# Performance work log

Hardware: AMD Instinct MI355X
Metric: run time of the kernel (lower is better)

The kernel has to match this reference:

```python
import jax, jax.numpy as jnp
import numpy as np

T, X_D, M_N, CHUNK, REDUCE = 2048, 2048, 64, 64, 8
M_D = X_D // REDUCE          # 256
DECAY_D = M_D // 4           # 64
H_D = X_D * 2                # factor=2
FF_D = 256 * round(int(H_D * (2.0 / 3.0)) / 256)  # 2816


def setup_inputs() -> dict:
    key = jax.random.key(0)
    ks = jax.random.split(key, 20)
    def lin(k, out_d, in_d):
        return (jax.random.normal(k, (out_d, in_d), jnp.float32) / np.sqrt(in_d).astype(np.float32))
    return {
        "xs": jax.random.normal(ks[0], (T, X_D), jnp.float32),
        "attn_q": lin(ks[1], X_D // REDUCE, X_D),
        "attn_k": lin(ks[2], X_D // REDUCE, X_D // REDUCE),
        "attn_v": lin(ks[3], X_D, X_D),
        "attn_o": lin(ks[4], X_D, X_D),
        "attn_r": lin(ks[5], X_D, X_D),
        "mem_f": lin(ks[6], M_N, X_D),
        "mem_q": lin(ks[7], M_D, X_D),
        "mem_k": lin(ks[8], M_D, M_D),
        "mem_v": lin(ks[9], M_D, X_D),
        "mem_o": lin(ks[10], X_D, M_D),
        "mem_r": lin(ks[11], X_D, X_D),
        "mem_beta": -jnp.ones((M_N, M_D), jnp.float32),
        "mem_decay": 3.0 * jnp.ones((M_N, DECAY_D), jnp.float32),
        "mem_l": jax.random.uniform(ks[12], (M_N, M_D), dtype=jnp.float32),
        "ff_in1": lin(ks[13], FF_D, X_D),
        "ff_in2": lin(ks[14], FF_D, X_D),
        "ff_out": lin(ks[15], X_D, FF_D),
        "sn1_g": jnp.sqrt(jnp.float32(X_D)),
        "sn2_g": jnp.sqrt(jnp.float32(X_D)),
    }


def _rotate_half(x):
    x1 = x[..., ::2]
    x2 = x[..., 1::2]
    return jnp.stack((-x2, x1), axis=-1).reshape(x.shape)


def _scale_norm(x, g):
    return x * (g / (jnp.linalg.norm(x, axis=-1, keepdims=True) + 1e-8))


def _attn(xs, Wq, Wk, Wv, Wo, Wr):
    n = CHUNK
    q = xs @ Wq.T                       # (T, dk)
    k = q @ Wk.T                        # k is computed from q (as in source)
    v = xs @ Wv.T                       # (T, x_d)
    c = xs.shape[0] // n
    dk = q.shape[-1]
    q = q.reshape(c, n, dk)
    k = k.reshape(c, n, dk)
    v = v.reshape(c, n, v.shape[-1])

    def with_prev(a):                   # prepend previous chunk (zero for chunk 0)
        prev = jnp.concatenate([jnp.zeros_like(a[:1]), a[:-1]], axis=0)
        return jnp.concatenate([prev, a], axis=1)   # (c, 2n, d)

    k2, v2 = with_prev(k), with_prev(v)

    # RoPE over 2n key positions; queries take the last n positions
    inv_freq = 1.0 / (10000.0 ** (jnp.arange(0, dk, 2, dtype=jnp.float32) / dk))
    ang = jnp.arange(2 * n, dtype=jnp.float32)[:, None] * inv_freq[None, :]
    sin = jnp.repeat(jnp.sin(ang), 2, axis=-1)      # (2n, dk) interleaved
    cos = jnp.repeat(jnp.cos(ang), 2, axis=-1)
    q = q * cos[None, n:] + _rotate_half(q) * sin[None, n:]
    k2 = k2 * cos[None] + _rotate_half(k2) * sin[None]

    qk = jnp.einsum('cnk,cmk->cnm', q, k2) / jnp.sqrt(jnp.float32(dk))
    allowed = jnp.arange(2 * n)[None, :] <= (jnp.arange(n)[:, None] + n)  # tril offset n
    A = jax.nn.softmax(jnp.where(allowed[None], qk, -jnp.inf), axis=-1)
    y = jnp.einsum('cnm,cmv->cnv', A, v2).reshape(xs.shape[0], -1)
    return (y @ Wo.T) * jax.nn.sigmoid(xs @ Wr.T)


def _mem(xs, Wf, Wq, Wk, Wv, Wo, Wr, beta_p, decay_p, l_p):
    v = xs @ Wv.T                                       # (T, m_d)
    f = jax.nn.sigmoid(xs @ Wf.T)[:, :, None]           # (T, m_n, 1)
    beta = jax.nn.sigmoid(beta_p)[None]                 # (1, m_n, m_d)
    gamma = jnp.concatenate(
        [jnp.ones((M_N, M_D - DECAY_D), xs.dtype), jax.nn.sigmoid(decay_p)], axis=1
    )[None]                                             # (1, m_n, m_d)
    ws = (1.0 - f * beta) * gamma                       # (T, m_n, m_d)
    fvs = f * v[:, None, :]                             # (T, m_n, m_d)

    def bin_assoc(ei, ej):
        ai, bi = ei
        aj, bj = ej
        return (aj * ai, aj * bi + bj)

    _, mems = jax.lax.associative_scan(bin_assoc, (ws, fvs), axis=0)  # (T, m_n, m_d)

    q = xs @ Wq.T                                       # (T, m_d)
    k = jnp.einsum('nmd,kd->nmk', mems, Wk) + l_p[None]
    A = jax.nn.softmax(jnp.einsum('nmk,nk->nm', k, q) / jnp.sqrt(jnp.float32(M_D)), axis=-1)
    y = jnp.einsum('nm,nmd->nd', A, mems)
    return (y @ Wo.T) * jax.nn.sigmoid(xs @ Wr.T)


def _ff(xs, W1, W2, Wo):
    return (jax.nn.silu(xs @ W1.T) * (xs @ W2.T)) @ Wo.T


def reference(xs, attn_q, attn_k, attn_v, attn_o, attn_r,
              mem_f, mem_q, mem_k, mem_v, mem_o, mem_r,
              mem_beta, mem_decay, mem_l,
              ff_in1, ff_in2, ff_out, sn1_g, sn2_g):
    xn = _scale_norm(xs, sn1_g)
    xs = (_attn(xn, attn_q, attn_k, attn_v, attn_o, attn_r)
          + _mem(xn, mem_f, mem_q, mem_k, mem_v, mem_o, mem_r, mem_beta, mem_decay, mem_l)
          + xs)
    xs = _ff(_scale_norm(xs, sn2_g), ff_in1, ff_in2, ff_out) + xs
    return xs
```

## Files before the change

### kernel.cpp

```cpp
#include <hip/hip_runtime.h>
#include <math.h>


typedef short bhalf8 __attribute__((ext_vector_type(8)));
typedef float f32x4 __attribute__((ext_vector_type(4)));

#define CC_LD 7168
#define COL_V   0
#define COL_B1  2048
#define COL_B2  4096
#define COL_QB  6144
#define COL_VM  6400
#define COL_QM  6656
#define COL_FG  6912

#define AS1 __attribute__((address_space(1)))
#define AS3 __attribute__((address_space(3)))

__device__ __forceinline__ float sigmoidf_(float x){ return 1.0f/(1.0f+expf(-x)); }

__device__ __forceinline__ unsigned short f2b(float f){
  unsigned u = __float_as_uint(f);
  unsigned r = (u + 0x7fffu + ((u>>16)&1u)) >> 16;
  return (unsigned short)r;
}
__device__ __forceinline__ float b2f(unsigned short h){
  return __uint_as_float(((unsigned)h)<<16);
}

__global__ void k_f2b_all(
    const float* __restrict__ av, const float* __restrict__ ar, const float* __restrict__ mr,
    const float* __restrict__ aq, const float* __restrict__ mv, const float* __restrict__ mq,
    const float* __restrict__ mf, const float* __restrict__ ao, const float* __restrict__ mo,
    const float* __restrict__ f1, const float* __restrict__ f2, const float* __restrict__ fo,
    const float* __restrict__ ak,
    unsigned short* __restrict__ WCAT, unsigned short* __restrict__ AOB,
    unsigned short* __restrict__ MOB, unsigned short* __restrict__ FFW,
    unsigned short* __restrict__ FFOB, unsigned short* __restrict__ AKB){
  int i = blockIdx.x*256 + threadIdx.x;
  const float* s; unsigned short* d; int off;
  if (i < 3571712){
    d = WCAT + (size_t)i*4;
    if      (i < 1048576){ s = av; off = i; }
    else if (i < 2097152){ s = ar; off = i-1048576; }
    else if (i < 3145728){ s = mr; off = i-2097152; }
    else if (i < 3276800){ s = aq; off = i-3145728; }
    else if (i < 3407872){ s = mv; off = i-3276800; }
    else if (i < 3538944){ s = mq; off = i-3407872; }
    else                 { s = mf; off = i-3538944; }
  }
  else if (i < 4620288){ off = i-3571712; s = ao; d = AOB  + (size_t)off*4; }
  else if (i < 4751360){ off = i-4620288; s = mo; d = MOB  + (size_t)off*4; }
  else if (i < 6193152){ off = i-4751360; s = f1;
    int row = off >> 9, c4 = off & 511;
    d = FFW + ((size_t)row*2)*2048 + c4*4; }
  else if (i < 7634944){ off = i-6193152; s = f2;
    int row = off >> 9, c4 = off & 511;
    d = FFW + ((size_t)row*2 + 1)*2048 + c4*4; }
  else if (i < 9076736){ off = i-7634944; s = fo; d = FFOB + (size_t)off*4; }
  else if (i < 9093120){ off = i-9076736; s = ak; d = AKB  + (size_t)off*4; }
  else return;
  float4 v = ((const float4*)s)[off];
  ushort4 o;
  o.x = f2b(v.x); o.y = f2b(v.y); o.z = f2b(v.z); o.w = f2b(v.w);
  *(ushort4*)d = o;
}

__global__ void k_f2bT(const float* __restrict__ s, unsigned short* __restrict__ d){
  int i = blockIdx.x, j = threadIdx.x;
  d[(size_t)j*256 + i] = f2b(s[(size_t)i*256 + j]);
}

__global__ void k_trig(float2* __restrict__ TR){
  int idx = blockIdx.x*256 + threadIdx.x;
  int pos = idx >> 7, j = idx & 127;
  float inv = powf(10000.f, -(float)j/128.f);
  float a = (float)pos * inv;
  TR[idx] = make_float2(cosf(a), sinf(a));
}

__global__ __launch_bounds__(256) void k_scalenorm_b(const float* __restrict__ x,
    const float* __restrict__ g, unsigned short* __restrict__ ob){
  int row = blockIdx.x, tid = threadIdx.x;
  const float* xr = x + (size_t)row*2048;
  float ss = 0.f;
  for (int j = tid; j < 2048; j += 256){ float v = xr[j]; ss += v*v; }
  __shared__ float red[256];
  red[tid] = ss; __syncthreads();
  for (int s = 128; s > 0; s >>= 1){ if (tid < s) red[tid] += red[tid+s]; __syncthreads(); }
  float scale = g[0] / (sqrtf(red[0]) + 1e-8f);
  unsigned short* orow = ob + (size_t)row*2048;
  for (int j4 = tid; j4 < 512; j4 += 256){
    float4 v = *(const float4*)(xr + j4*4);
    ushort4 o;
    o.x = f2b(v.x*scale); o.y = f2b(v.y*scale); o.z = f2b(v.z*scale); o.w = f2b(v.w*scale);
    ((ushort4*)orow)[j4] = o;
  }
}

__global__ __launch_bounds__(512) void k_gemm_big(
    const unsigned short* __restrict__ A, int lda,
    const unsigned short* __restrict__ B,
    unsigned short* __restrict__ Cb, int K, int ldc, int epi, int gate_ld){
  __shared__ unsigned short LDSu[49152];
  int tid = threadIdx.x;
  int w = tid >> 6, l = tid & 63;
  int bi = blockIdx.y, bj = blockIdx.x;
  int m0 = bi*256, n0 = bj*256;
  int wr = w >> 2, wc = w & 3;

  f32x4 acc[8][4];
#pragma unroll
  for (int i=0;i<8;++i)
#pragma unroll
    for (int j=0;j<4;++j){ f32x4 z = {0.f,0.f,0.f,0.f}; acc[i][j] = z; }

  const int r0 = tid >> 2;
  const int gsrc8 = (((tid&3) ^ ((tid>>3)&3)) * 8);

  auto stage = [&](int bs, int kt){
    unsigned short* db = LDSu + bs*16384;
    const unsigned short* ap0 = A + (size_t)(m0 + r0)*lda       + kt*32 + gsrc8;
    const unsigned short* ap1 = A + (size_t)(m0 + 128 + r0)*lda + kt*32 + gsrc8;
    const unsigned short* bp0 = B + (size_t)(n0 + r0)*K         + kt*32 + gsrc8;
    const unsigned short* bp1 = B + (size_t)(n0 + 128 + r0)*K   + kt*32 + gsrc8;
    __builtin_amdgcn_global_load_lds((const AS1 void*)ap0, (AS3 void*)(db + tid*8),         16, 0, 0);
    __builtin_amdgcn_global_load_lds((const AS1 void*)ap1, (AS3 void*)(db + 4096 + tid*8),  16, 0, 0);
    __builtin_amdgcn_global_load_lds((const AS1 void*)bp0, (AS3 void*)(db + 8192 + tid*8),  16, 0, 0);
    __builtin_amdgcn_global_load_lds((const AS1 void*)bp1, (AS3 void*)(db + 12288 + tid*8), 16, 0, 0);
  };

  const int nt = K >> 5;
  stage(0, 0);
  stage(1, 1);
  asm volatile("s_waitcnt vmcnt(4)" ::: "memory");
  __builtin_amdgcn_s_barrier();

  const int lr = l & 15;
  const int gsw = (((l>>4) ^ ((l>>1)&3)) * 8);
  const int aoff = (wr*128 + lr)*32 + gsw;
  const int boff = 8192 + (wc*64 + lr)*32 + gsw;

  int cur = 0;
  for (int t = 0; t < nt; ++t){
    if (t + 2 < nt) stage((t+2)%3, t+2);
    const unsigned short* Tb = LDSu + cur*16384;
    bhalf8 bfr[4];
#pragma unroll
    for (int n=0;n<4;++n) bfr[n] = *(const bhalf8*)(Tb + boff + n*512);
    __builtin_amdgcn_s_setprio(1);
#pragma unroll
    for (int fr=0;fr<8;++fr){
      bhalf8 af = *(const bhalf8*)(Tb + aoff + fr*512);
#pragma unroll
      for (int n=0;n<4;++n)
        acc[fr][n] = __builtin_amdgcn_mfma_f32_16x16x32_bf16(af, bfr[n], acc[fr][n], 0, 0, 0);
    }
    __builtin_amdgcn_s_setprio(0);
    if (t + 1 < nt){
      if (t + 2 < nt){ asm volatile("s_waitcnt vmcnt(4)" ::: "memory"); }
      else           { asm volatile("s_waitcnt vmcnt(0)" ::: "memory"); }
      __builtin_amdgcn_s_barrier();
      cur = (cur == 2) ? 0 : cur + 1;
    }
  }

#pragma unroll
  for (int fr=0;fr<8;++fr){
    int rowb = m0 + wr*128 + fr*16 + ((l>>4)<<2);
#pragma unroll
    for (int r=0;r<4;++r){
      int row = rowb + r;
      size_t rbase = (size_t)row*ldc;
      size_t gbase = (size_t)row*gate_ld;
#pragma unroll
      for (int n=0;n<4;++n){
        int col = n0 + wc*64 + n*16 + (l&15);
        float v = acc[fr][n][r];
        if (epi == 4){
          float o = __shfl_xor(v, 1);
          if ((l & 1) == 0)
            Cb[gbase + (col>>1)] = f2b(v*sigmoidf_(v)*o);
        } else {
          Cb[rbase + col] = f2b(v);
        }
      }
    }
  }
}

__global__ __launch_bounds__(256) void k_gemm_p(
    const unsigned short* __restrict__ A, int lda,
    const unsigned short* __restrict__ B,
    float* __restrict__ C, unsigned short* __restrict__ Cb,
    int N, int K, int ldc, int epi,
    const float* __restrict__ add,
    const unsigned short* __restrict__ gate, int gate_ld,
    const unsigned short* A2, const unsigned short* B2, float* C2){
  __shared__ unsigned short LDSu[24576];
  int tid = threadIdx.x;
  int w = tid >> 6, l = tid & 63;
  int bi = blockIdx.y, bj = blockIdx.x;
  const unsigned short* Ap = A; const unsigned short* Bp = B; float* Cp = C;
  if (blockIdx.z){ Ap = A2; Bp = B2; Cp = C2; }
  int m0 = bi*128, n0 = bj*128;
  int wr = w >> 1, wc = w & 1;

  f32x4 acc[4][4];
#pragma unroll
  for (int i=0;i<4;++i)
#pragma unroll
    for (int j=0;j<4;++j){ f32x4 z = {0.f,0.f,0.f,0.f}; acc[i][j] = z; }

  const int r0 = tid >> 2;
  const int gsrc8 = (((tid&3) ^ ((tid>>3)&3)) * 8);

  auto stage = [&](int bs, int kt){
    unsigned short* db = LDSu + bs*8192;
    const unsigned short* ap0 = Ap + (size_t)(m0 + r0)*lda      + kt*32 + gsrc8;
    const unsigned short* ap1 = Ap + (size_t)(m0 + 64 + r0)*lda + kt*32 + gsrc8;
    const unsigned short* bp0 = Bp + (size_t)(n0 + r0)*K        + kt*32 + gsrc8;
    const unsigned short* bp1 = Bp + (size_t)(n0 + 64 + r0)*K   + kt*32 + gsrc8;
    __builtin_amdgcn_global_load_lds((const AS1 void*)ap0, (AS3 void*)(db + tid*8),        16, 0, 0);
    __builtin_amdgcn_global_load_lds((const AS1 void*)ap1, (AS3 void*)(db + 2048 + tid*8), 16, 0, 0);
    __builtin_amdgcn_global_load_lds((const AS1 void*)bp0, (AS3 void*)(db + 4096 + tid*8), 16, 0, 0);
    __builtin_amdgcn_global_load_lds((const AS1 void*)bp1, (AS3 void*)(db + 6144 + tid*8), 16, 0, 0);
  };

  const int nt = K >> 5;
  stage(0, 0);
  stage(1, 1);
  asm volatile("s_waitcnt vmcnt(4)" ::: "memory");
  __builtin_amdgcn_s_barrier();

  const int lr = l & 15;
  const int gsw = (((l>>4) ^ ((l>>1)&3)) * 8);
  const int aoff = (wr*64 + lr)*32 + gsw;
  const int boff = 4096 + (wc*64 + lr)*32 + gsw;

  int cur = 0;
  for (int t = 0; t < nt; ++t){
    if (t + 2 < nt) stage((t+2)%3, t+2);
    const unsigned short* Tb = LDSu + cur*8192;
    bhalf8 af[4], bfr[4];
#pragma unroll
    for (int m=0;m<4;++m) af[m]  = *(const bhalf8*)(Tb + aoff + m*512);
#pragma unroll
    for (int n=0;n<4;++n) bfr[n] = *(const bhalf8*)(Tb + boff + n*512);
    __builtin_amdgcn_s_setprio(1);
#pragma unroll
    for (int m=0;m<4;++m)
#pragma unroll
      for (int n=0;n<4;++n)
        acc[m][n] = __builtin_amdgcn_mfma_f32_16x16x32_bf16(af[m], bfr[n], acc[m][n], 0, 0, 0);
    __builtin_amdgcn_s_setprio(0);
    if (t + 1 < nt){
      if (t + 2 < nt){ asm volatile("s_waitcnt vmcnt(4)" ::: "memory"); }
      else           { asm volatile("s_waitcnt vmcnt(0)" ::: "memory"); }
      __builtin_amdgcn_s_barrier();
      cur = (cur == 2) ? 0 : cur + 1;
    }
  }

#pragma unroll
  for (int m=0;m<4;++m){
    int rowb = m0 + wr*64 + m*16 + ((l>>4)<<2);
#pragma unroll
    for (int r=0;r<4;++r){
      int row = rowb + r;
      size_t rbase = (size_t)row*ldc;
      size_t gbase = (size_t)row*gate_ld;
#pragma unroll
      for (int n=0;n<4;++n){
        int col = n0 + wc*64 + n*16 + (l&15);
        float v = acc[m][n][r];
        if (add) v += add[rbase + col];
        if (epi == 2) v *= sigmoidf_(b2f(gate[gbase + col]));
        if (epi == 3) Cb[rbase + col] = f2b(v);
        else          Cp[rbase + col] = v;
      }
    }
  }
}

__global__ __launch_bounds__(256) void k_gemm_fuse2(
    const unsigned short* __restrict__ A,  const unsigned short* __restrict__ B,
    const unsigned short* __restrict__ A2, const unsigned short* __restrict__ B2,
    const unsigned short* __restrict__ gate1, const unsigned short* __restrict__ gate2,
    const float* __restrict__ xs, float* __restrict__ XS2){
  __shared__ unsigned short LDSu[24576];
  int tid = threadIdx.x;
  int w = tid >> 6, l = tid & 63;
  int bi = blockIdx.y, bj = blockIdx.x;
  int m0 = bi*128, n0 = bj*128;
  int wr = w >> 1, wc = w & 1;

  f32x4 acc[4][4], acc2[4][4];
#pragma unroll
  for (int i=0;i<4;++i)
#pragma unroll
    for (int j=0;j<4;++j){ f32x4 z = {0.f,0.f,0.f,0.f}; acc[i][j] = z; acc2[i][j] = z; }

  const int r0 = tid >> 2;
  const int gsrc8 = (((tid&3) ^ ((tid>>3)&3)) * 8);

  auto stage = [&](int bs, int kt, const unsigned short* Ap, int lda,
                   const unsigned short* Bp, int ldb){
    unsigned short* db = LDSu + bs*8192;
    const unsigned short* ap0 = Ap + (size_t)(m0 + r0)*lda      + kt*32 + gsrc8;
    const unsigned short* ap1 = Ap + (size_t)(m0 + 64 + r0)*lda + kt*32 + gsrc8;
    const unsigned short* bp0 = Bp + (size_t)(n0 + r0)*ldb      + kt*32 + gsrc8;
    const unsigned short* bp1 = Bp + (size_t)(n0 + 64 + r0)*ldb + kt*32 + gsrc8;
    __builtin_amdgcn_global_load_lds((const AS1 void*)ap0, (AS3 void*)(db + tid*8),        16, 0, 0);
    __builtin_amdgcn_global_load_lds((const AS1 void*)ap1, (AS3 void*)(db + 2048 + tid*8), 16, 0, 0);
    __builtin_amdgcn_global_load_lds((const AS1 void*)bp0, (AS3 void*)(db + 4096 + tid*8), 16, 0, 0);
    __builtin_amdgcn_global_load_lds((const AS1 void*)bp1, (AS3 void*)(db + 6144 + tid*8), 16, 0, 0);
  };

  const int lr = l & 15;
  const int gsw = (((l>>4) ^ ((l>>1)&3)) * 8);
  const int aoff = (wr*64 + lr)*32 + gsw;
  const int boff = 4096 + (wc*64 + lr)*32 + gsw;

  {
    const int nt = 64;
    stage(0, 0, A, 2048, B, 2048);
    stage(1, 1, A, 2048, B, 2048);
    asm volatile("s_waitcnt vmcnt(4)" ::: "memory");
    __builtin_amdgcn_s_barrier();
    int cur = 0;
    for (int t = 0; t < nt; ++t){
      if (t + 2 < nt) stage((t+2)%3, t+2, A, 2048, B, 2048);
      const unsigned short* Tb = LDSu + cur*8192;
      bhalf8 af[4], bfr[4];
#pragma unroll
      for (int m=0;m<4;++m) af[m]  = *(const bhalf8*)(Tb + aoff + m*512);
#pragma unroll
      for (int n=0;n<4;++n) bfr[n] = *(const bhalf8*)(Tb + boff + n*512);
      __builtin_amdgcn_s_setprio(1);
#pragma unroll
      for (int m=0;m<4;++m)
#pragma unroll
        for (int n=0;n<4;++n)
          acc[m][n] = __builtin_amdgcn_mfma_f32_16x16x32_bf16(af[m], bfr[n], acc[m][n], 0, 0, 0);
      __builtin_amdgcn_s_setprio(0);
      if (t + 1 < nt){
        if (t + 2 < nt){ asm volatile("s_waitcnt vmcnt(4)" ::: "memory"); }
        else           { asm volatile("s_waitcnt vmcnt(0)" ::: "memory"); }
        __builtin_amdgcn_s_barrier();
        cur = (cur == 2) ? 0 : cur + 1;
      }
    }
  }
  __syncthreads();

  {
    const int nt = 8;
    stage(0, 0, A2, 256, B2, 256);
    stage(1, 1, A2, 256, B2, 256);
    asm volatile("s_waitcnt vmcnt(4)" ::: "memory");
    __builtin_amdgcn_s_barrier();
    int cur = 0;
    for (int t = 0; t < nt; ++t){
      if (t + 2 < nt) stage((t+2)%3, t+2, A2, 256, B2, 256);
      const unsigned short* Tb = LDSu + cur*8192;
      bhalf8 af[4], bfr[4];
#pragma unroll
      for (int m=0;m<4;++m) af[m]  = *(const bhalf8*)(Tb + aoff + m*512);
#pragma unroll
      for (int n=0;n<4;++n) bfr[n] = *(const bhalf8*)(Tb + boff + n*512);
      __builtin_amdgcn_s_setprio(1);
#pragma unroll
      for (int m=0;m<4;++m)
#pragma unroll
        for (int n=0;n<4;++n)
          acc2[m][n] = __builtin_amdgcn_mfma_f32_16x16x32_bf16(af[m], bfr[n], acc2[m][n], 0, 0, 0);
      __builtin_amdgcn_s_setprio(0);
      if (t + 1 < nt){
        if (t + 2 < nt){ asm volatile("s_waitcnt vmcnt(4)" ::: "memory"); }
        else           { asm volatile("s_waitcnt vmcnt(0)" ::: "memory"); }
        __builtin_amdgcn_s_barrier();
        cur = (cur == 2) ? 0 : cur + 1;
      }
    }
  }

#pragma unroll
  for (int m=0;m<4;++m){
    int rowb = m0 + wr*64 + m*16 + ((l>>4)<<2);
#pragma unroll
    for (int r=0;r<4;++r){
      int row = rowb + r;
      size_t gb = (size_t)row*CC_LD;
      size_t rb = (size_t)row*2048;
#pragma unroll
      for (int n=0;n<4;++n){
        int col = n0 + wc*64 + n*16 + (l&15);
        float v = acc[m][n][r]*sigmoidf_(b2f(gate1[gb + col]))
                + acc2[m][n][r]*sigmoidf_(b2f(gate2[gb + col]))
                + xs[rb + col];
        XS2[rb + col] = v;
      }
    }
  }
}

__global__ __launch_bounds__(256) void k_attn_scores_mfma(
    const unsigned short* __restrict__ CCqb, const float* __restrict__ K0,
    const float2* __restrict__ TR, unsigned short* __restrict__ P){
  __shared__ unsigned short Ks[128*256];
  int c = blockIdx.x, tid = threadIdx.x;
  for (int it = 0; it < 16; ++it){
    int id = tid + it*256;
    int m = id >> 5;
    int cs = (id & 31) * 8;
    float v[8];
    if (c == 0 && m < 64){
#pragma unroll
      for (int u=0;u<8;++u) v[u] = 0.f;
    } else {
      int gr = (c-1)*64 + m;
      const float* kr = K0 + (size_t)gr*256 + cs;
      float4 x0 = *(const float4*)kr, x1 = *(const float4*)(kr+4);
      v[0]=x0.x; v[1]=x0.y; v[2]=x0.z; v[3]=x0.w;
      v[4]=x1.x; v[5]=x1.y; v[6]=x1.z; v[7]=x1.w;
#pragma unroll
      for (int p2=0;p2<4;++p2){
        float2 t = TR[m*128 + (cs>>1) + p2];
        float e = v[2*p2], o = v[2*p2+1];
        v[2*p2]   = e*t.x - o*t.y;
        v[2*p2+1] = o*t.x + e*t.y;
      }
    }
    unsigned short pk[8];
#pragma unroll
    for (int u=0;u<8;++u) pk[u] = f2b(v[u]);
    int byte = m*512 + ((cs*2) ^ ((m&7)<<4));
    *(bhalf8*)((char*)&Ks[0] + byte) = *(const bhalf8*)pk;
  }
  __syncthreads();

  int w = tid >> 6, l = tid & 63;
  int lr = l & 15, lkg = l >> 4;
  f32x4 acc[8];
#pragma unroll
  for (int n=0;n<8;++n){ f32x4 z = {0.f,0.f,0.f,0.f}; acc[n] = z; }

  int iq = w*16 + lr;
  const unsigned short* qbase = CCqb + (size_t)(c*64 + iq)*CC_LD;
  int pos = 64 + iq;

  for (int kt = 0; kt < 8; ++kt){
    int k0c = kt*32 + lkg*8;
    bhalf8 q8 = *(const bhalf8*)(qbase + k0c);
    float v[8];
#pragma unroll
    for (int u=0;u<8;++u) v[u] = b2f((unsigned short)(((short*)&q8)[u]));
#pragma unroll
    for (int p2=0;p2<4;++p2){
      float2 t = TR[pos*128 + (k0c>>1) + p2];
      float e = v[2*p2], o = v[2*p2+1];
      v[2*p2]   = e*t.x - o*t.y;
      v[2*p2+1] = o*t.x + e*t.y;
    }
    unsigned short pk[8];
#pragma unroll
    for (int u=0;u<8;++u) pk[u] = f2b(v[u]);
    bhalf8 af = *(const bhalf8*)pk;
#pragma unroll
    for (int n=0;n<8;++n){
      int m = n*16 + lr;
      int byte = m*512 + ((k0c*2) ^ ((m&7)<<4));
      bhalf8 bf = *(const bhalf8*)((const char*)&Ks[0] + byte);
      acc[n] = __builtin_amdgcn_mfma_f32_16x16x32_bf16(af, bf, acc[n], 0, 0, 0);
    }
  }

  int i0 = w*16 + lkg*4;
  float mx[4] = {-1e30f,-1e30f,-1e30f,-1e30f};
  float sm[4] = {0.f,0.f,0.f,0.f};
#pragma unroll
  for (int n=0;n<8;++n){
    int col = n*16 + lr;
#pragma unroll
    for (int r=0;r<4;++r){
      float vv = acc[n][r] * (1.f/16.f);
      if (col > i0 + r + 64) vv = -1e30f;
      acc[n][r] = vv;
      mx[r] = fmaxf(mx[r], vv);
    }
  }
#pragma unroll
  for (int s=1; s<16; s<<=1)
#pragma unroll
    for (int r=0;r<4;++r) mx[r] = fmaxf(mx[r], __shfl_xor(mx[r], s));
#pragma unroll
  for (int n=0;n<8;++n)
#pragma unroll
    for (int r=0;r<4;++r){
      float e = expf(acc[n][r] - mx[r]);
      acc[n][r] = e; sm[r] += e;
    }
#pragma unroll
  for (int s=1; s<16; s<<=1)
#pragma unroll
    for (int r=0;r<4;++r) sm[r] += __shfl_xor(sm[r], s);
  float rcp[4];
#pragma unroll
  for (int r=0;r<4;++r) rcp[r] = 1.f/sm[r];

  unsigned short* Pr = P + (size_t)c*8192;
#pragma unroll
  for (int n=0;n<8;++n){
    int col = n*16 + lr;
#pragma unroll
    for (int r=0;r<4;++r)
      Pr[(i0+r)*128 + col] = f2b(acc[n][r]*rcp[r]);
  }
}

__global__ __launch_bounds__(256) void k_attn_pv_mfma(
    const unsigned short* __restrict__ P, const unsigned short* __restrict__ Vb, int vld,
    unsigned short* __restrict__ Y){
  __shared__ unsigned short Vt[128*128];
  int ct = blockIdx.x, c = blockIdx.y, tid = threadIdx.x;
  {
    int k = tid >> 1;
    int ch = (tid & 1) * 64;
    if (c == 0 && k < 64){
      for (int u=0; u<64; ++u){
        int col = ch + u;
        int byte = col*256 + ((k*2) ^ ((col&7)<<4));
        *(unsigned short*)((char*)&Vt[0] + byte) = 0;
      }
    } else {
      int gr = (c-1)*64 + k;
      const unsigned short* vr = Vb + (size_t)gr*vld + ct*128 + ch;
      for (int u8=0; u8<8; ++u8){
        bhalf8 x = *(const bhalf8*)(vr + u8*8);
#pragma unroll
        for (int u=0;u<8;++u){
          int col = ch + u8*8 + u;
          int byte = col*256 + ((k*2) ^ ((col&7)<<4));
          *(unsigned short*)((char*)&Vt[0] + byte) = (unsigned short)(((short*)&x)[u]);
        }
      }
    }
  }
  __syncthreads();
  int w = tid >> 6, l = tid & 63, lr = l & 15, lkg = l >> 4;
  f32x4 acc[8];
#pragma unroll
  for (int n=0;n<8;++n){ f32x4 z = {0.f,0.f,0.f,0.f}; acc[n] = z; }
  const unsigned short* Pr = P + (size_t)c*8192;
  for (int kt=0; kt<4; ++kt){
    int kb = kt*32 + lkg*8;
    bhalf8 af = *(const bhalf8*)(Pr + (w*16 + lr)*128 + kb);
#pragma unroll
    for (int n=0;n<8;++n){
      int col = n*16 + lr;
      int byte = col*256 + ((kb*2) ^ ((col&7)<<4));
      bhalf8 bf = *(const bhalf8*)((const char*)&Vt[0] + byte);
      acc[n] = __builtin_amdgcn_mfma_f32_16x16x32_bf16(af, bf, acc[n], 0, 0, 0);
    }
  }
  int row0 = c*64 + w*16 + lkg*4;
#pragma unroll
  for (int n=0;n<8;++n){
    int col = ct*128 + n*16 + lr;
#pragma unroll
    for (int r=0;r<4;++r)
      Y[(size_t)(row0+r)*2048 + col] = f2b(acc[n][r]);
  }
}

__global__ __launch_bounds__(256) void k_scan1(const unsigned short* __restrict__ CC,
    const float* __restrict__ beta_p, const float* __restrict__ decay_p,
    float* __restrict__ CP, float* __restrict__ CQ){
  int c = blockIdx.x, mg = blockIdx.y, d = threadIdx.x;
  __shared__ float Fs[512];
  for (int v = threadIdx.x; v < 512; v += 256){
    int s = v >> 3, j = v & 7;
    Fs[v] = sigmoidf_(b2f(CC[(size_t)(c*64+s)*CC_LD + COL_FG + mg*8 + j]));
  }
  __syncthreads();
  float beta[8], gamma[8], Pa[8], Qa[8];
#pragma unroll
  for (int j=0;j<8;++j){
    int m = mg*8+j;
    beta[j]  = sigmoidf_(beta_p[m*256+d]);
    gamma[j] = (d < 192) ? 1.f : sigmoidf_(decay_p[m*64 + (d-192)]);
    Pa[j] = 1.f; Qa[j] = 0.f;
  }
  for (int s = 0; s < 64; ++s){
    float vm = b2f(CC[(size_t)(c*64+s)*CC_LD + COL_VM + d]);
#pragma unroll
    for (int j=0;j<8;++j){
      float f = Fs[s*8+j];
      float w = (1.f - f*beta[j])*gamma[j];
      Pa[j] *= w;
      Qa[j] = w*Qa[j] + f*vm;
    }
  }
#pragma unroll
  for (int j=0;j<8;++j){
    size_t idx = ((size_t)c*64 + mg*8 + j)*256 + d;
    CP[idx] = Pa[j]; CQ[idx] = Qa[j];
  }
}

__global__ __launch_bounds__(256) void k_scan2(const float* __restrict__ CP,
    const float* __restrict__ CQ, float* __restrict__ SIN){
  int m = blockIdx.x, d = threadIdx.x;
  float S = 0.f;
  for (int c = 0; c < 32; ++c){
    size_t idx = ((size_t)c*64 + m)*256 + d;
    SIN[idx] = S;
    S = CP[idx]*S + CQ[idx];
  }
}

__global__ __launch_bounds__(256) void k_scan3(const unsigned short* __restrict__ CC,
    const float* __restrict__ beta_p, const float* __restrict__ decay_p,
    const float* __restrict__ SIN, unsigned short* __restrict__ MEMS){
  int c = blockIdx.x, mg = blockIdx.y, d = threadIdx.x;
  __shared__ float Fs[512];
  for (int v = threadIdx.x; v < 512; v += 256){
    int s = v >> 3, j = v & 7;
    Fs[v] = sigmoidf_(b2f(CC[(size_t)(c*64+s)*CC_LD + COL_FG + mg*8 + j]));
  }
  __syncthreads();
  float beta[8], gamma[8], S[8];
#pragma unroll
  for (int j=0;j<8;++j){
    int m = mg*8+j;
    beta[j]  = sigmoidf_(beta_p[m*256+d]);
    gamma[j] = (d < 192) ? 1.f : sigmoidf_(decay_p[m*64 + (d-192)]);
    S[j] = SIN[((size_t)c*64 + m)*256 + d];
  }
  for (int s = 0; s < 64; ++s){
    float vm = b2f(CC[(size_t)(c*64+s)*CC_LD + COL_VM + d]);
    size_t tb = (size_t)(c*64+s)*64;
#pragma unroll
    for (int j=0;j<8;++j){
      float f = Fs[s*8+j];
      float w = (1.f - f*beta[j])*gamma[j];
      S[j] = w*S[j] + f*vm;
      MEMS[(tb + mg*8 + j)*256 + d] = f2b(S[j]);
    }
  }
}

__global__ __launch_bounds__(256) void k_memread(const unsigned short* __restrict__ MEMS,
    const float* __restrict__ QH, const unsigned short* __restrict__ QMs, int qm_ld,
    const float* __restrict__ L, unsigned short* __restrict__ YMb){
  int t = blockIdx.x, tid = threadIdx.x;
  int wave = tid >> 6, lane = tid & 63;
  __shared__ float anorm[64];
  const unsigned short* Mt = MEMS + (size_t)t*16384;
  float4 qh4 = *(const float4*)(QH + (size_t)t*256 + lane*4);
  ushort4 qmu = *(const ushort4*)(QMs + (size_t)t*qm_ld + lane*4);
  float qm0 = b2f(qmu.x), qm1 = b2f(qmu.y), qm2 = b2f(qmu.z), qm3 = b2f(qmu.w);
  for (int mi = 0; mi < 16; ++mi){
    int m = wave*16 + mi;
    ushort4 su = *(const ushort4*)(Mt + m*256 + lane*4);
    float4 l4 = *(const float4*)(L + (size_t)m*256 + lane*4);
    float p = b2f(su.x)*qh4.x + b2f(su.y)*qh4.y + b2f(su.z)*qh4.z + b2f(su.w)*qh4.w
            + l4.x*qm0 + l4.y*qm1 + l4.z*qm2 + l4.w*qm3;
#pragma unroll
    for (int off = 32; off > 0; off >>= 1) p += __shfl_down(p, off);
    if (lane == 0) anorm[m] = p * (1.f/16.f);
  }
  __syncthreads();
  if (tid < 64){
    float v = anorm[tid];
    float mx = v;
#pragma unroll
    for (int off = 32; off > 0; off >>= 1) mx = fmaxf(mx, __shfl_xor(mx, off));
    float e = expf(v - mx);
    float s = e;
#pragma unroll
    for (int off = 32; off > 0; off >>= 1) s += __shfl_xor(s, off);
    anorm[tid] = e / s;
  }
  __syncthreads();
  float acc = 0.f;
  for (int m = 0; m < 64; ++m) acc += anorm[m]*b2f(Mt[m*256 + tid]);
  YMb[(size_t)t*256 + tid] = f2b(acc);
}

extern "C" void kernel_launch(void* const* d_in, const int* in_sizes, int n_in,
                              void* d_out, int out_size, void* d_ws, size_t ws_size,
                              hipStream_t stream){
  const float* xs        = (const float*)d_in[0];
  const float* attn_q    = (const float*)d_in[1];
  const float* attn_k    = (const float*)d_in[2];
  const float* attn_v    = (const float*)d_in[3];
  const float* attn_o    = (const float*)d_in[4];
  const float* attn_r    = (const float*)d_in[5];
  const float* mem_f     = (const float*)d_in[6];
  const float* mem_q     = (const float*)d_in[7];
  const float* mem_k     = (const float*)d_in[8];
  const float* mem_v     = (const float*)d_in[9];
  const float* mem_o     = (const float*)d_in[10];
  const float* mem_r     = (const float*)d_in[11];
  const float* mem_beta  = (const float*)d_in[12];
  const float* mem_decay = (const float*)d_in[13];
  const float* mem_l     = (const float*)d_in[14];
  const float* ff1       = (const float*)d_in[15];
  const float* ff2       = (const float*)d_in[16];
  const float* ffo       = (const float*)d_in[17];
  const float* sn1       = (const float*)d_in[18];
  const float* sn2       = (const float*)d_in[19];
  float* out = (float*)d_out;
  float* W = (float*)d_ws;

  unsigned short* XNb  = (unsigned short*)(W + 0);
  unsigned short* WCAT = (unsigned short*)(W + 2097152);
  unsigned short* CCb  = (unsigned short*)(W + 9437184);
  unsigned short* AOB  = (unsigned short*)(W + 16777216);
  unsigned short* MOB  = (unsigned short*)(W + 18874368);
  unsigned short* FFW  = (unsigned short*)(W + 19136512);
  unsigned short* FFOB = (unsigned short*)(W + 24903680);
  unsigned short* AKB  = (unsigned short*)(W + 27787264);
  unsigned short* MKTB = (unsigned short*)(W + 27820032);
  unsigned short* Ybb  = (unsigned short*)(W + 27852800);
  float*          XS2  = W + 34144256;
  unsigned short* MEMSb= (unsigned short*)(W + 38338560);
  float*          CP   = W + 55115776;
  float*          CQ   = W + 55640064;
  float*          SIN  = W + 56164352;
  float2*         TRIG = (float2*)(W + 0);
  float*          K0   = W + 32768;
  unsigned short* P    = (unsigned short*)(W + 557056);
  float*          QH   = W + 688128;
  unsigned short* YMb  = (unsigned short*)(W + 1212416);
  unsigned short* XN2b = MEMSb;
  unsigned short* H1b  = (unsigned short*)(W + 40435712);

  dim3 blk(256);
  dim3 blk512(512);

  k_f2b_all<<<dim3(35520), blk, 0, stream>>>(attn_v, attn_r, mem_r, attn_q, mem_v, mem_q,
      mem_f, attn_o, mem_o, ff1, ff2, ffo, attn_k, WCAT, AOB, MOB, FFW, FFOB, AKB);
  k_f2bT<<<dim3(256), blk, 0, stream>>>(mem_k, MKTB);

  k_scalenorm_b<<<dim3(2048), blk, 0, stream>>>(xs, sn1, XNb);

  k_gemm_big<<<dim3(28, 8), blk512, 0, stream>>>(XNb, 2048, WCAT, CCb, 2048, CC_LD, 3, 0);

  k_trig<<<dim3(64), blk, 0, stream>>>(TRIG);

  k_gemm_p<<<dim3(2, 16, 2), blk, 0, stream>>>(CCb + COL_QB, CC_LD, AKB, K0, nullptr, 256, 256, 256, 0,
      nullptr, nullptr, 0, CCb + COL_QM, MKTB, QH);

  k_attn_scores_mfma<<<dim3(32), blk, 0, stream>>>(CCb + COL_QB, K0, TRIG, P);
  k_attn_pv_mfma<<<dim3(16, 32), blk, 0, stream>>>(P, CCb + COL_V, CC_LD, Ybb);

  k_scan1<<<dim3(32, 8), blk, 0, stream>>>(CCb, mem_beta, mem_decay, CP, CQ);
  k_scan2<<<dim3(64), blk, 0, stream>>>(CP, CQ, SIN);
  k_scan3<<<dim3(32, 8), blk, 0, stream>>>(CCb, mem_beta, mem_decay, SIN, MEMSb);
  k_memread<<<dim3(2048), blk, 0, stream>>>(MEMSb, QH, CCb + COL_QM, CC_LD, mem_l, YMb);

  k_gemm_fuse2<<<dim3(16, 16), blk, 0, stream>>>(Ybb, AOB, YMb, MOB,
      CCb + COL_B1, CCb + COL_B2, xs, XS2);

  k_scalenorm_b<<<dim3(2048), blk, 0, stream>>>(XS2, sn2, XN2b);

  k_gemm_big<<<dim3(22, 8), blk512, 0, stream>>>(XN2b, 2048, FFW, H1b, 2048, 5632, 4, 2816);
  k_gemm_p<<<dim3(16, 16), blk, 0, stream>>>(H1b, 2816, FFOB, out, nullptr, 2048, 2816, 2048, 0,
      XS2, nullptr, 0, nullptr, nullptr, nullptr);
}
```

Baseline: 421.6 us.

## Split GEMM K-step into two phases interleaving A/B prefetch with MFMA halves

Splits each K-iteration of the bf16 MFMA GEMM into two halves. Each half loads a group of A fragments from LDS, issues either the A or the B global-to-LDS prefetch for tile t+2, then runs 16 MFMAs. The aim is to spread global load issue between compute phases, in the style of a ping-pong schedule. It adds three extra workgroup barriers per iteration, which may cost more than the overlap it gains.

```diff
diff --git a/kernel.cpp b/kernel.cpp
--- a/kernel.cpp
+++ b/kernel.cpp
@@ -118,21 +118,24 @@
   const int r0 = tid >> 2;
   const int gsrc8 = (((tid&3) ^ ((tid>>3)&3)) * 8);
 
-  auto stage = [&](int bs, int kt){
+  auto stage_a = [&](int bs, int kt){
     unsigned short* db = LDSu + bs*16384;
     const unsigned short* ap0 = A + (size_t)(m0 + r0)*lda       + kt*32 + gsrc8;
     const unsigned short* ap1 = A + (size_t)(m0 + 128 + r0)*lda + kt*32 + gsrc8;
+    __builtin_amdgcn_global_load_lds((const AS1 void*)ap0, (AS3 void*)(db + tid*8),        16, 0, 0);
+    __builtin_amdgcn_global_load_lds((const AS1 void*)ap1, (AS3 void*)(db + 4096 + tid*8), 16, 0, 0);
+  };
+  auto stage_b = [&](int bs, int kt){
+    unsigned short* db = LDSu + bs*16384;
     const unsigned short* bp0 = B + (size_t)(n0 + r0)*K         + kt*32 + gsrc8;
     const unsigned short* bp1 = B + (size_t)(n0 + 128 + r0)*K   + kt*32 + gsrc8;
-    __builtin_amdgcn_global_load_lds((const AS1 void*)ap0, (AS3 void*)(db + tid*8),         16, 0, 0);
-    __builtin_amdgcn_global_load_lds((const AS1 void*)ap1, (AS3 void*)(db + 4096 + tid*8),  16, 0, 0);
     __builtin_amdgcn_global_load_lds((const AS1 void*)bp0, (AS3 void*)(db + 8192 + tid*8),  16, 0, 0);
     __builtin_amdgcn_global_load_lds((const AS1 void*)bp1, (AS3 void*)(db + 12288 + tid*8), 16, 0, 0);
   };
 
   const int nt = K >> 5;
-  stage(0, 0);
-  stage(1, 1);
+  stage_a(0, 0); stage_b(0, 0);
+  stage_a(1, 1); stage_b(1, 1);
   asm volatile("s_waitcnt vmcnt(4)" ::: "memory");
   __builtin_amdgcn_s_barrier();
 
@@ -143,19 +146,33 @@
 
   int cur = 0;
   for (int t = 0; t < nt; ++t){
-    if (t + 2 < nt) stage((t+2)%3, t+2);
     const unsigned short* Tb = LDSu + cur*16384;
-    bhalf8 bfr[4];
+    bhalf8 bfr[4], af0[4];
 #pragma unroll
     for (int n=0;n<4;++n) bfr[n] = *(const bhalf8*)(Tb + boff + n*512);
+#pragma unroll
+    for (int m=0;m<4;++m) af0[m] = *(const bhalf8*)(Tb + aoff + m*512);
+    if (t + 2 < nt) stage_a((t+2)%3, t+2);
+    __builtin_amdgcn_s_barrier();
     __builtin_amdgcn_s_setprio(1);
 #pragma unroll
-    for (int fr=0;fr<8;++fr){
-      bhalf8 af = *(const bhalf8*)(Tb + aoff + fr*512);
+    for (int m=0;m<4;++m)
 #pragma unroll
       for (int n=0;n<4;++n)
-        acc[fr][n] = __builtin_amdgcn_mfma_f32_16x16x32_bf16(af, bfr[n], acc[fr][n], 0, 0, 0);
-    }
+        acc[m][n] = __builtin_amdgcn_mfma_f32_16x16x32_bf16(af0[m], bfr[n], acc[m][n], 0, 0, 0);
+    __builtin_amdgcn_s_setprio(0);
+    __builtin_amdgcn_s_barrier();
+    bhalf8 af1[4];
+#pragma unroll
+    for (int m=0;m<4;++m) af1[m] = *(const bhalf8*)(Tb + aoff + (m+4)*512);
+    if (t + 2 < nt) stage_b((t+2)%3, t+2);
+    __builtin_amdgcn_s_barrier();
+    __builtin_amdgcn_s_setprio(1);
+#pragma unroll
+    for (int m=0;m<4;++m)
+#pragma unroll
+      for (int n=0;n<4;++n)
+        acc[m+4][n] = __builtin_amdgcn_mfma_f32_16x16x32_bf16(af1[m], bfr[n], acc[m+4][n], 0, 0, 0);
     __builtin_amdgcn_s_setprio(0);
     if (t + 1 < nt){
       if (t + 2 < nt){ asm volatile("s_waitcnt vmcnt(4)" ::: "memory"); }
```

New measurement: 429.0 us. No clear change (+1.8%).

## Replace 256x256 GEMM tiles with 128x128 tiles and add XCD-aware block swizzle

Applied to the files above, without the earlier changes.

Removes the 512-thread 256x256 big-tile GEMM and runs the fused QKV/gate projection and the FF in1/in2 SiLU GEMM with 256-thread 128x128 tiles instead. A new dedicated SiLU-gated kernel takes over the FF case. The launch grids grow fourfold, so more workgroups fill the CUs. A block-index swizzle that groups consecutive tiles onto the same XCD is added to the 128-tile GEMMs to improve L2 locality. In exchange, smaller tiles mean less data reuse per block and more global traffic.

```diff
diff --git a/kernel.cpp b/kernel.cpp
--- a/kernel.cpp
+++ b/kernel.cpp
@@ -26,6 +26,15 @@
 }
 __device__ __forceinline__ float b2f(unsigned short h){
   return __uint_as_float(((unsigned)h)<<16);
+}
+
+__device__ __forceinline__ void xcd_swz(int& bi, int& bj){
+  int gx = gridDim.x;
+  int nwg = gx * gridDim.y;
+  int lin = blockIdx.y * gx + blockIdx.x;
+  int q = nwg >> 3;
+  int swz = (lin & 7) * q + (lin >> 3);
+  bj = swz % gx; bi = swz / gx;
 }
 
 __global__ void k_f2b_all(
@@ -98,97 +107,6 @@
   }
 }
 
-__global__ __launch_bounds__(512) void k_gemm_big(
-    const unsigned short* __restrict__ A, int lda,
-    const unsigned short* __restrict__ B,
-    unsigned short* __restrict__ Cb, int K, int ldc, int epi, int gate_ld){
-  __shared__ unsigned short LDSu[49152];
-  int tid = threadIdx.x;
-  int w = tid >> 6, l = tid & 63;
-  int bi = blockIdx.y, bj = blockIdx.x;
-  int m0 = bi*256, n0 = bj*256;
-  int wr = w >> 2, wc = w & 3;
-
-  f32x4 acc[8][4];
-#pragma unroll
-  for (int i=0;i<8;++i)
-#pragma unroll
-    for (int j=0;j<4;++j){ f32x4 z = {0.f,0.f,0.f,0.f}; acc[i][j] = z; }
-
-  const int r0 = tid >> 2;
-  const int gsrc8 = (((tid&3) ^ ((tid>>3)&3)) * 8);
-
-  auto stage = [&](int bs, int kt){
-    unsigned short* db = LDSu + bs*16384;
-    const unsigned short* ap0 = A + (size_t)(m0 + r0)*lda       + kt*32 + gsrc8;
-    const unsigned short* ap1 = A + (size_t)(m0 + 128 + r0)*lda + kt*32 + gsrc8;
-    const unsigned short* bp0 = B + (size_t)(n0 + r0)*K         + kt*32 + gsrc8;
-    const unsigned short* bp1 = B + (size_t)(n0 + 128 + r0)*K   + kt*32 + gsrc8;
-    __builtin_amdgcn_global_load_lds((const AS1 void*)ap0, (AS3 void*)(db + tid*8),         16, 0, 0);
-    __builtin_amdgcn_global_load_lds((const AS1 void*)ap1, (AS3 void*)(db + 4096 + tid*8),  16, 0, 0);
-    __builtin_amdgcn_global_load_lds((const AS1 void*)bp0, (AS3 void*)(db + 8192 + tid*8),  16, 0, 0);
-    __builtin_amdgcn_global_load_lds((const AS1 void*)bp1, (AS3 void*)(db + 12288 + tid*8), 16, 0, 0);
-  };
-
-  const int nt = K >> 5;
-  stage(0, 0);
-  stage(1, 1);
-  asm volatile("s_waitcnt vmcnt(4)" ::: "memory");
-  __builtin_amdgcn_s_barrier();
-
-  const int lr = l & 15;
-  const int gsw = (((l>>4) ^ ((l>>1)&3)) * 8);
-  const int aoff = (wr*128 + lr)*32 + gsw;
-  const int boff = 8192 + (wc*64 + lr)*32 + gsw;
-
-  int cur = 0;
-  for (int t = 0; t < nt; ++t){
-    if (t + 2 < nt) stage((t+2)%3, t+2);
-    const unsigned short* Tb = LDSu + cur*16384;
-    bhalf8 bfr[4];
-#pragma unroll
-    for (int n=0;n<4;++n) bfr[n] = *(const bhalf8*)(Tb + boff + n*512);
-    __builtin_amdgcn_s_setprio(1);
-#pragma unroll
-    for (int fr=0;fr<8;++fr){
-      bhalf8 af = *(const bhalf8*)(Tb + aoff + fr*512);
-#pragma unroll
-      for (int n=0;n<4;++n)
-        acc[fr][n] = __builtin_amdgcn_mfma_f32_16x16x32_bf16(af, bfr[n], acc[fr][n], 0, 0, 0);
-    }
-    __builtin_amdgcn_s_setprio(0);
-    if (t + 1 < nt){
-      if (t + 2 < nt){ asm volatile("s_waitcnt vmcnt(4)" ::: "memory"); }
-      else           { asm volatile("s_waitcnt vmcnt(0)" ::: "memory"); }
-      __builtin_amdgcn_s_barrier();
-      cur = (cur == 2) ? 0 : cur + 1;
-    }
-  }
-
-#pragma unroll
-  for (int fr=0;fr<8;++fr){
-    int rowb = m0 + wr*128 + fr*16 + ((l>>4)<<2);
-#pragma unroll
-    for (int r=0;r<4;++r){
-      int row = rowb + r;
-      size_t rbase = (size_t)row*ldc;
-      size_t gbase = (size_t)row*gate_ld;
-#pragma unroll
-      for (int n=0;n<4;++n){
-        int col = n0 + wc*64 + n*16 + (l&15);
-        float v = acc[fr][n][r];
-        if (epi == 4){
-          float o = __shfl_xor(v, 1);
-          if ((l & 1) == 0)
-            Cb[gbase + (col>>1)] = f2b(v*sigmoidf_(v)*o);
-        } else {
-          Cb[rbase + col] = f2b(v);
-        }
-      }
-    }
-  }
-}
-
 __global__ __launch_bounds__(256) void k_gemm_p(
     const unsigned short* __restrict__ A, int lda,
     const unsigned short* __restrict__ B,
@@ -200,7 +118,7 @@
   __shared__ unsigned short LDSu[24576];
   int tid = threadIdx.x;
   int w = tid >> 6, l = tid & 63;
-  int bi = blockIdx.y, bj = blockIdx.x;
+  int bi, bj; xcd_swz(bi, bj);
   const unsigned short* Ap = A; const unsigned short* Bp = B; float* Cp = C;
   if (blockIdx.z){ Ap = A2; Bp = B2; Cp = C2; }
   int m0 = bi*128, n0 = bj*128;
@@ -283,6 +201,92 @@
   }
 }
 
+__global__ __launch_bounds__(256) void k_gemm_silu(
+    const unsigned short* __restrict__ A, int lda,
+    const unsigned short* __restrict__ B,
+    unsigned short* __restrict__ Cb, int K, int out_ld){
+  __shared__ unsigned short LDSu[24576];
+  int tid = threadIdx.x;
+  int w = tid >> 6, l = tid & 63;
+  int bi, bj; xcd_swz(bi, bj);
+  int m0 = bi*128, n0 = bj*128;
+  int wr = w >> 1, wc = w & 1;
+
+  f32x4 acc[4][4];
+#pragma unroll
+  for (int i=0;i<4;++i)
+#pragma unroll
+    for (int j=0;j<4;++j){ f32x4 z = {0.f,0.f,0.f,0.f}; acc[i][j] = z; }
+
+  const int r0 = tid >> 2;
+  const int gsrc8 = (((tid&3) ^ ((tid>>3)&3)) * 8);
+
+  auto stage = [&](int bs, int kt){
+    unsigned short* db = LDSu + bs*8192;
+    const unsigned short* ap0 = A + (size_t)(m0 + r0)*lda      + kt*32 + gsrc8;
+    const unsigned short* ap1 = A + (size_t)(m0 + 64 + r0)*lda + kt*32 + gsrc8;
+    const unsigned short* bp0 = B + (size_t)(n0 + r0)*K        + kt*32 + gsrc8;
+    const unsigned short* bp1 = B + (size_t)(n0 + 64 + r0)*K   + kt*32 + gsrc8;
+    __builtin_amdgcn_global_load_lds((const AS1 void*)ap0, (AS3 void*)(db + tid*8),        16, 0, 0);
+    __builtin_amdgcn_global_load_lds((const AS1 void*)ap1, (AS3 void*)(db + 2048 + tid*8), 16, 0, 0);
+    __builtin_amdgcn_global_load_lds((const AS1 void*)bp0, (AS3 void*)(db + 4096 + tid*8), 16, 0, 0);
+    __builtin_amdgcn_global_load_lds((const AS1 void*)bp1, (AS3 void*)(db + 6144 + tid*8), 16, 0, 0);
+  };
+
+  const int nt = K >> 5;
+  stage(0, 0);
+  stage(1, 1);
+  asm volatile("s_waitcnt vmcnt(4)" ::: "memory");
+  __builtin_amdgcn_s_barrier();
+
+  const int lr = l & 15;
+  const int gsw = (((l>>4) ^ ((l>>1)&3)) * 8);
+  const int aoff = (wr*64 + lr)*32 + gsw;
+  const int boff = 4096 + (wc*64 + lr)*32 + gsw;
+
+  int cur = 0;
+  for (int t = 0; t < nt; ++t){
+    if (t + 2 < nt) stage((t+2)%3, t+2);
+    const unsigned short* Tb = LDSu + cur*8192;
+    bhalf8 af[4], bfr[4];
+#pragma unroll
+    for (int m=0;m<4;++m) af[m]  = *(const bhalf8*)(Tb + aoff + m*512);
+#pragma unroll
+    for (int n=0;n<4;++n) bfr[n] = *(const bhalf8*)(Tb + boff + n*512);
+    __builtin_amdgcn_s_setprio(1);
+#pragma unroll
+    for (int m=0;m<4;++m)
+#pragma unroll
+      for (int n=0;n<4;++n)
+        acc[m][n] = __builtin_amdgcn_mfma_f32_16x16x32_bf16(af[m], bfr[n], acc[m][n], 0, 0, 0);
+    __builtin_amdgcn_s_setprio(0);
+    if (t + 1 < nt){
+      if (t + 2 < nt){ asm volatile("s_waitcnt vmcnt(4)" ::: "memory"); }
+      else           { asm volatile("s_waitcnt vmcnt(0)" ::: "memory"); }
+      __builtin_amdgcn_s_barrier();
+      cur = (cur == 2) ? 0 : cur + 1;
+    }
+  }
+
+#pragma unroll
+  for (int m=0;m<4;++m){
+    int rowb = m0 + wr*64 + m*16 + ((l>>4)<<2);
+#pragma unroll
+    for (int r=0;r<4;++r){
+      int row = rowb + r;
+      size_t gbase = (size_t)row*out_ld;
+#pragma unroll
+      for (int n=0;n<4;++n){
+        int col = n0 + wc*64 + n*16 + (l&15);
+        float v = acc[m][n][r];
+        float o = __shfl_xor(v, 1);
+        if ((l & 1) == 0)
+          Cb[gbase + (col>>1)] = f2b(v*sigmoidf_(v)*o);
+      }
+    }
+  }
+}
+
 __global__ __launch_bounds__(256) void k_gemm_fuse2(
     const unsigned short* __restrict__ A,  const unsigned short* __restrict__ B,
     const unsigned short* __restrict__ A2, const unsigned short* __restrict__ B2,
@@ -291,7 +295,7 @@
   __shared__ unsigned short LDSu[24576];
   int tid = threadIdx.x;
   int w = tid >> 6, l = tid & 63;
-  int bi = blockIdx.y, bj = blockIdx.x;
+  int bi, bj; xcd_swz(bi, bj);
   int m0 = bi*128, n0 = bj*128;
   int wr = w >> 1, wc = w & 1;
 
@@ -739,7 +743,6 @@
   unsigned short* H1b  = (unsigned short*)(W + 40435712);
 
   dim3 blk(256);
-  dim3 blk512(512);
 
   k_f2b_all<<<dim3(35520), blk, 0, stream>>>(attn_v, attn_r, mem_r, attn_q, mem_v, mem_q,
       mem_f, attn_o, mem_o, ff1, ff2, ffo, attn_k, WCAT, AOB, MOB, FFW, FFOB, AKB);
@@ -747,7 +750,8 @@
 
   k_scalenorm_b<<<dim3(2048), blk, 0, stream>>>(xs, sn1, XNb);
 
-  k_gemm_big<<<dim3(28, 8), blk512, 0, stream>>>(XNb, 2048, WCAT, CCb, 2048, CC_LD, 3, 0);
+  k_gemm_p<<<dim3(56, 16), blk, 0, stream>>>(XNb, 2048, WCAT, nullptr, CCb, CC_LD, 2048, CC_LD, 3,
+      nullptr, nullptr, 0, nullptr, nullptr, nullptr);
 
   k_trig<<<dim3(64), blk, 0, stream>>>(TRIG);
 
@@ -767,7 +771,7 @@
 
   k_scalenorm_b<<<dim3(2048), blk, 0, stream>>>(XS2, sn2, XN2b);
 
-  k_gemm_big<<<dim3(22, 8), blk512, 0, stream>>>(XN2b, 2048, FFW, H1b, 2048, 5632, 4, 2816);
+  k_gemm_silu<<<dim3(44, 16), blk, 0, stream>>>(XN2b, 2048, FFW, H1b, 2048, 2816);
   k_gemm_p<<<dim3(16, 16), blk, 0, stream>>>(H1b, 2816, FFOB, out, nullptr, 2048, 2816, 2048, 0,
       XS2, nullptr, 0, nullptr, nullptr, nullptr);
 }
```

Measured after the change: 420.3 us. About the same (-0.3%).
